# Performance work log

Hardware: AMD Instinct MI355X
Metric: run time of the kernel (lower is better)

The kernel has to match this reference:

```python
import jax, jax.numpy as jnp
import numpy as np
import math

B, S, D = 2, 2048, 512
H = 8
DEPTH = D // H
MAX_REL = 1024
NEG_INF = -1.0e9


def skew(t):
    # t: (..., r, c). Pad a zero column on the left, reshape to move relative
    # logits into their absolute positions (Music Transformer skew trick).
    r, c = t.shape[-2], t.shape[-1]
    padded = jnp.pad(t, [(0, 0)] * (t.ndim - 1) + [(1, 0)])
    s = padded.reshape(-1, c + 1, r)[:, 1:]
    return s.reshape(t.shape)


def setup_inputs() -> dict:
    key = jax.random.key(0)
    ks = jax.random.split(key, 12)
    sc = 1.0 / math.sqrt(D)
    return {
        "q": jax.random.normal(ks[0], (B, S, D), jnp.float32),
        "k": jax.random.normal(ks[1], (B, S, D), jnp.float32),
        "v": jax.random.normal(ks[2], (B, S, D), jnp.float32),
        "mask": jax.random.randint(ks[3], (B, 1, S, S), 0, 2, jnp.int32),
        "Wq_w": jax.random.normal(ks[4], (D, D), jnp.float32) * sc,
        "Wq_b": jnp.zeros((D,), jnp.float32),
        "Wk_w": jax.random.normal(ks[5], (D, D), jnp.float32) * sc,
        "Wk_b": jnp.zeros((D,), jnp.float32),
        "Wv_w": jax.random.normal(ks[6], (D, D), jnp.float32) * sc,
        "Wv_b": jnp.zeros((D,), jnp.float32),
        "E": jax.random.normal(ks[7], (MAX_REL, D), jnp.float32),
        "Wo_w": jax.random.normal(ks[8], (D, D), jnp.float32) * sc,
        "Wo_b": jnp.zeros((D,), jnp.float32),
    }


def reference(q, k, v, mask, Wq_w, Wq_b, Wk_w, Wk_b, Wv_w, Wv_b, E, Wo_w, Wo_b):
    # Linear projections (torch Linear: x @ W^T + b)
    qp = q @ Wq_w.T + Wq_b
    kp = k @ Wk_w.T + Wk_b
    vp = v @ Wv_w.T + Wv_b

    # Required relative position embeddings for seq_len S (S >= MAX_REL here:
    # repeat E[0] for the first S-MAX_REL positions, then the full table).
    n_rep = max(0, S - MAX_REL)
    e = jnp.concatenate([jnp.tile(E[0:1], (n_rep, 1)), E[max(0, MAX_REL - S):]], axis=0)  # (S, D)

    # Split heads: (B,S,D)->(B,H,S,depth); e: (S,D)->(H,S,depth)
    qh = qp.reshape(B, S, H, DEPTH).transpose(0, 2, 1, 3)
    kh = kp.reshape(B, S, H, DEPTH).transpose(0, 2, 1, 3)
    vh = vp.reshape(B, S, H, DEPTH).transpose(0, 2, 1, 3)
    eh = e.reshape(S, H, DEPTH).transpose(1, 0, 2)

    QKt = jnp.einsum('bhqd,bhkd->bhqk', qh, kh)
    Srel = skew(jnp.einsum('bhqd,hkd->bhqk', qh, eh))
    logits = (QKt + Srel) / math.sqrt(DEPTH)
    logits = logits + mask.astype(logits.dtype) * NEG_INF
    attn = jnp.einsum('bhqk,bhkd->bhqd', jax.nn.softmax(logits, axis=-1), vh)

    # Merge heads and output projection
    out = attn.transpose(0, 2, 1, 3).reshape(B, S, D)
    return out @ Wo_w.T + Wo_b
```

## Files before the change

### kernel.cpp

```cpp
#include <hip/hip_runtime.h>
#include <hip/hip_bf16.h>

#define BB 2
#define SS 2048
#define DD 512
#define HH 8
#define DP 64
#define MR 1024

typedef __attribute__((ext_vector_type(8))) short bf16x8;
typedef __attribute__((ext_vector_type(4))) float floatx4;

static __device__ __forceinline__ unsigned short f2b(float x) {
    __hip_bfloat16 h = __float2bfloat16(x);
    return *reinterpret_cast<unsigned short*>(&h);
}
static __device__ __forceinline__ float b2f(unsigned short u) {
    __hip_bfloat16 h = *reinterpret_cast<__hip_bfloat16*>(&u);
    return __bfloat162float(h);
}
static __device__ __forceinline__ unsigned int cvtpk(float lo, float hi) {
    unsigned int r;
    asm("v_cvt_pk_bf16_f32 %0, %1, %2" : "=v"(r) : "v"(lo), "v"(hi));
    return r;
}
static __device__ __forceinline__ void gll16(const void* g, void* l) {
    __builtin_amdgcn_global_load_lds(
        (const __attribute__((address_space(1))) void*)g,
        (__attribute__((address_space(3))) void*)l, 16, 0, 0);
}
static __device__ __forceinline__ int xoff(int ks, int quad, int row) {
    return (((ks * 4 + quad) ^ (row & 7)) * 16);
}

__global__ __launch_bounds__(256) void prep_kernel(
    const float* __restrict__ Wq, const float* __restrict__ Wk,
    const float* __restrict__ Wv, const float* __restrict__ Wo,
    const float* __restrict__ E,  const float* __restrict__ q,
    const float* __restrict__ k,  const float* __restrict__ v,
    const int* __restrict__ mask,
    unsigned short* __restrict__ Wqb, unsigned short* __restrict__ Wkb,
    unsigned short* __restrict__ Wvb, unsigned short* __restrict__ Wob,
    unsigned short* __restrict__ Eb,  unsigned short* __restrict__ qb16,
    unsigned short* __restrict__ kb16, unsigned short* __restrict__ vb16,
    unsigned long long* __restrict__ bits)
{
    const int blk = blockIdx.x;
    if (blk < 7680) {
        const int gid = blk * 256 + threadIdx.x;
        const float* src; unsigned short* dst; int off;
        if      (gid < 65536)   { src = Wq; dst = Wqb;  off = gid; }
        else if (gid < 131072)  { src = Wk; dst = Wkb;  off = gid - 65536; }
        else if (gid < 196608)  { src = Wv; dst = Wvb;  off = gid - 131072; }
        else if (gid < 262144)  { src = Wo; dst = Wob;  off = gid - 196608; }
        else if (gid < 393216)  { src = E;  dst = Eb;   off = gid - 262144; }
        else if (gid < 917504)  { src = q;  dst = qb16; off = gid - 393216; }
        else if (gid < 1441792) { src = k;  dst = kb16; off = gid - 917504; }
        else                    { src = v;  dst = vb16; off = gid - 1441792; }
        float4 x = ((const float4*)src)[off];
        ushort4 u; u.x = f2b(x.x); u.y = f2b(x.y); u.z = f2b(x.z); u.w = f2b(x.w);
        ((ushort4*)dst)[off] = u;
    } else {
        const size_t wid = (size_t)(blk - 7680) * 4 + (threadIdx.x >> 6);
        const int lane = threadIdx.x & 63;
        const int mv = mask[wid * 64 + lane];
        unsigned long long bal = __ballot(mv != 0);
        if (lane == 0) bits[wid] = bal;
    }
}

static __device__ __forceinline__ void gemm64_main(
    const unsigned short* __restrict__ A, const unsigned short* __restrict__ Wb,
    char* AsB, char* WsB, int m0, int n0,
    const int srow[2], const int scol[2],
    int w, int quad, int l15, int wm, int wn,
    floatx4 acc[2][2])
{
    for (int k0 = 0; k0 < 512; k0 += 64) {
        if (k0) __syncthreads();
#pragma unroll
        for (int i = 0; i < 2; i++) {
            gll16(A + (size_t)(m0 + srow[i]) * 512 + k0 + scol[i] * 8,
                  AsB + (w * 2 + i) * 1024);
            gll16(Wb + (size_t)(n0 + srow[i]) * 512 + k0 + scol[i] * 8,
                  WsB + (w * 2 + i) * 1024);
        }
        __syncthreads();
#pragma unroll
        for (int ks = 0; ks < 2; ks++) {
            bf16x8 a[2], bb[2];
#pragma unroll
            for (int mi = 0; mi < 2; mi++) {
                const int row = wm * 32 + mi * 16 + l15;
                a[mi] = *(const bf16x8*)(AsB + row * 128 + xoff(ks, quad, row));
            }
#pragma unroll
            for (int ni = 0; ni < 2; ni++) {
                const int row = wn * 32 + ni * 16 + l15;
                bb[ni] = *(const bf16x8*)(WsB + row * 128 + xoff(ks, quad, row));
            }
#pragma unroll
            for (int mi = 0; mi < 2; mi++)
#pragma unroll
                for (int ni = 0; ni < 2; ni++)
                    acc[mi][ni] = __builtin_amdgcn_mfma_f32_16x16x32_bf16(
                        a[mi], bb[ni], acc[mi][ni], 0, 0, 0);
        }
    }
}

__global__ __launch_bounds__(256) void gemm_proj(
    const unsigned short* __restrict__ Xq, const unsigned short* __restrict__ Xk,
    const unsigned short* __restrict__ Xv,
    const unsigned short* __restrict__ Wqb, const unsigned short* __restrict__ Wkb,
    const unsigned short* __restrict__ Wvb,
    const float* __restrict__ bq, const float* __restrict__ bk,
    const float* __restrict__ bv,
    const unsigned short* __restrict__ Eb,
    unsigned short* __restrict__ qp, unsigned short* __restrict__ kp,
    unsigned short* __restrict__ vpT, unsigned short* __restrict__ G)
{
    const int z = blockIdx.z;
    __shared__ __align__(16) char parena[27648];
    char* AsB = parena;
    char* WsB = parena + 8192;
    const int t = threadIdx.x, lane = t & 63, w = t >> 6;
    const int quad = lane >> 4, l15 = lane & 15;
    const int wm = w >> 1, wn = w & 1;
    const int m0 = blockIdx.x * 64, n0 = blockIdx.y * 64;

    int srow[2], scol[2];
#pragma unroll
    for (int i = 0; i < 2; i++) {
        const int p = (w * 2 + i) * 64 + lane;
        srow[i] = p >> 3; scol[i] = (p & 7) ^ (srow[i] & 7);
    }

    floatx4 acc[2][2];
#pragma unroll
    for (int mi = 0; mi < 2; mi++)
#pragma unroll
        for (int ni = 0; ni < 2; ni++)
            acc[mi][ni] = (floatx4){0.f, 0.f, 0.f, 0.f};

    if (z == 1) {
        gemm64_main(Xk, Wkb, AsB, WsB, m0, n0, srow, scol, w, quad, l15, wm, wn, acc);
#pragma unroll
        for (int ni = 0; ni < 2; ni++) {
            const int n = n0 + wn * 32 + ni * 16 + l15;
            const float bvl = bk[n];
#pragma unroll
            for (int mi = 0; mi < 2; mi++)
#pragma unroll
                for (int r = 0; r < 4; r++) {
                    const size_t m = (size_t)(m0 + wm * 32 + mi * 16 + quad * 4 + r);
                    kp[m * 512 + n] = f2b(acc[mi][ni][r] + bvl);
                }
        }
        __syncthreads();
#pragma unroll
        for (int mi = 0; mi < 2; mi++)
#pragma unroll
            for (int ni = 0; ni < 2; ni++)
                acc[mi][ni] = (floatx4){0.f, 0.f, 0.f, 0.f};
        gemm64_main(Xv, Wvb, AsB, WsB, m0, n0, srow, scol, w, quad, l15, wm, wn, acc);
        __syncthreads();
        unsigned short* Ls = (unsigned short*)parena;
#pragma unroll
        for (int ni = 0; ni < 2; ni++) {
            const int dcol = wn * 32 + ni * 16 + l15;
            const float bvl = bv[n0 + dcol];
#pragma unroll
            for (int mi = 0; mi < 2; mi++)
#pragma unroll
                for (int r = 0; r < 4; r++) {
                    const int srw = wm * 32 + mi * 16 + quad * 4 + r;
                    Ls[dcol * 72 + srw] = f2b(acc[mi][ni][r] + bvl);
                }
        }
        __syncthreads();
        const int bb2 = blockIdx.x >> 5, s0 = (blockIdx.x & 31) * 64, hh = blockIdx.y;
        const int drow = t >> 2, sc8 = (t & 3) * 8;
#pragma unroll
        for (int half = 0; half < 2; half++) {
            *(uint4*)&vpT[((size_t)(bb2 * 8 + hh) * 64 + drow) * SS + s0 + half * 32 + sc8] =
                *(const uint4*)&Ls[drow * 72 + half * 32 + sc8];
        }
    } else {
        gemm64_main(Xq, Wqb, AsB, WsB, m0, n0, srow, scol, w, quad, l15, wm, wn, acc);
        __syncthreads();
        unsigned short* Ls = (unsigned short*)parena;
#pragma unroll
        for (int ni = 0; ni < 2; ni++) {
            const int ch = wn * 32 + ni * 16 + l15;
            const float bvl = bq[n0 + ch];
#pragma unroll
            for (int mi = 0; mi < 2; mi++)
#pragma unroll
                for (int r = 0; r < 4; r++)
                    Ls[(wm * 32 + mi * 16 + quad * 4 + r) * 72 + ch] =
                        f2b(acc[mi][ni][r] + bvl);
        }
        __syncthreads();
        {
            const int row = t >> 2, c16 = (t & 3) * 16;
            const unsigned short* ls = &Ls[row * 72 + c16];
            unsigned short* qdst = &qp[(size_t)(m0 + row) * 512 + n0 + c16];
            *(uint4*)qdst = *(const uint4*)ls;
            *(uint4*)(qdst + 8) = *(const uint4*)(ls + 8);
        }
        bf16x8 af0 = *(const bf16x8*)&Ls[(w * 16 + l15) * 72 + quad * 8];
        bf16x8 af1 = *(const bf16x8*)&Ls[(w * 16 + l15) * 72 + 32 + quad * 8];

        const int bblk = m0 >> 11;
        const int i0 = m0 & 2047;
        const size_t grow0 = (size_t)(bblk * 8 + blockIdx.y) * SS + i0;
        char* EbL = parena + 10240;
        unsigned short* Gtw = (unsigned short*)(parena + 18432 + w * 2304);

        const int orow = lane >> 2, oseg = lane & 3;

        for (int tc = 0; tc < 16; tc++) {
            if (tc) __syncthreads();
#pragma unroll
            for (int i = 0; i < 2; i++)
                gll16(Eb + (size_t)(tc * 64 + srow[i]) * 512 + n0 + scol[i] * 8,
                      EbL + (w * 2 + i) * 1024);
            __syncthreads();
#pragma unroll
            for (int tt = 0; tt < 4; tt++) {
                const int row = tt * 16 + l15;
                bf16x8 b0 = *(const bf16x8*)(EbL + row * 128 + xoff(0, quad, row));
                bf16x8 b1 = *(const bf16x8*)(EbL + row * 128 + xoff(1, quad, row));
                floatx4 a2 = (floatx4){0.f, 0.f, 0.f, 0.f};
                a2 = __builtin_amdgcn_mfma_f32_16x16x32_bf16(af0, b0, a2, 0, 0, 0);
                a2 = __builtin_amdgcn_mfma_f32_16x16x32_bf16(af1, b1, a2, 0, 0, 0);
#pragma unroll
                for (int r = 0; r < 4; r++)
                    Gtw[(quad * 4 + r) * 72 + tt * 16 + l15] = f2b(a2[r]);
            }
            const unsigned short* gsrc = &Gtw[orow * 72 + oseg * 16];
            unsigned short* gdst = &G[(grow0 + w * 16 + orow) * MR + tc * 64 + oseg * 16];
            *(uint4*)gdst = *(const uint4*)gsrc;
            *(uint4*)(gdst + 8) = *(const uint4*)(gsrc + 8);
        }
    }
}

__global__ __launch_bounds__(256) void gemm_out(
    const unsigned short* __restrict__ A, const unsigned short* __restrict__ Wb,
    const float* __restrict__ bias, float* __restrict__ Out)
{
    __shared__ __align__(16) char parena[16384];
    char* AsB = parena;
    char* WsB = parena + 8192;
    const int t = threadIdx.x, lane = t & 63, w = t >> 6;
    const int quad = lane >> 4, l15 = lane & 15;
    const int wm = w >> 1, wn = w & 1;
    const int m0 = blockIdx.x * 64, n0 = blockIdx.y * 64;

    int srow[2], scol[2];
#pragma unroll
    for (int i = 0; i < 2; i++) {
        const int p = (w * 2 + i) * 64 + lane;
        srow[i] = p >> 3; scol[i] = (p & 7) ^ (srow[i] & 7);
    }

    floatx4 acc[2][2];
#pragma unroll
    for (int mi = 0; mi < 2; mi++)
#pragma unroll
        for (int ni = 0; ni < 2; ni++)
            acc[mi][ni] = (floatx4){0.f, 0.f, 0.f, 0.f};

    gemm64_main(A, Wb, AsB, WsB, m0, n0, srow, scol, w, quad, l15, wm, wn, acc);

#pragma unroll
    for (int ni = 0; ni < 2; ni++) {
        const int n = n0 + wn * 32 + ni * 16 + l15;
        const float bvl = bias[n];
#pragma unroll
        for (int mi = 0; mi < 2; mi++)
#pragma unroll
            for (int r = 0; r < 4; r++) {
                const size_t m = (size_t)(m0 + wm * 32 + mi * 16 + quad * 4 + r);
                Out[m * 512 + n] = acc[mi][ni][r] + bvl;
            }
    }
}

struct RelPF { ushort4 hi; ushort4 lo; int path; };

static __device__ __forceinline__ void rel_issue(
    const unsigned short* __restrict__ pdiag, int i0w, int k0, int quad,
    RelPF pf[2])
{
#pragma unroll
    for (int ct = 0; ct < 2; ct++) {
        const int k0c = k0 + ct * 16;
        const int gj0 = k0c + quad * 4;
        const int dmax = i0w + 15 - k0c;
        const int dmin = i0w - (k0c + 15);
        int path;
        if (dmin >= MR) path = 0;
        else if (dmin >= 0 && dmax <= MR - 1) path = 1;
        else if (dmax <= -2 && dmin >= -(MR + 1)) path = 2;
        else if (dmax <= -(MR + 2)) path = 3;
        else path = 4;
        pf[ct].path = path;
        if (path == 1 || path == 4) {
            const unsigned short* p = pdiag + 1023 + gj0;
            pf[ct].hi.x = p[0]; pf[ct].hi.y = p[1];
            pf[ct].hi.z = p[2]; pf[ct].hi.w = p[3];
        }
        if (path == 3 || path == 4) {
            const unsigned short* p = pdiag + max(gj0 - 2, 0);
            pf[ct].lo.x = p[0]; pf[ct].lo.y = p[1];
            pf[ct].lo.z = p[2]; pf[ct].lo.w = p[3];
        }
    }
}

static __device__ __forceinline__ void rel_convert(
    const RelPF& pf, int gi, int k0c, int quad,
    float d0a, float d0b, float relc[4])
{
    const int path = pf.path;
    if (path == 0) {
        relc[0] = relc[1] = relc[2] = relc[3] = d0a;
    } else if (path == 1) {
        relc[0] = b2f(pf.hi.x); relc[1] = b2f(pf.hi.y);
        relc[2] = b2f(pf.hi.z); relc[3] = b2f(pf.hi.w);
    } else if (path == 2) {
        relc[0] = relc[1] = relc[2] = relc[3] = d0b;
    } else if (path == 3) {
        relc[0] = b2f(pf.lo.x); relc[1] = b2f(pf.lo.y);
        relc[2] = b2f(pf.lo.z); relc[3] = b2f(pf.lo.w);
    } else {
        const int gj0 = k0c + quad * 4;
        const unsigned short hv[4] = {pf.hi.x, pf.hi.y, pf.hi.z, pf.hi.w};
        const unsigned short lv[4] = {pf.lo.x, pf.lo.y, pf.lo.z, pf.lo.w};
#pragma unroll
        for (int r = 0; r < 4; r++) {
            const int dd = gi - (gj0 + r);
            float rl;
            if (dd >= MR) rl = d0a;
            else if (dd >= 0) rl = b2f(hv[r]);
            else if (dd == -1) rl = 0.0f;
            else if (dd >= -(MR + 1)) rl = d0b;
            else rl = b2f(lv[r]);
            relc[r] = rl;
        }
    }
}

__global__ __launch_bounds__(256, 4) void attn_kernel(
    const unsigned short* __restrict__ qp, const unsigned short* __restrict__ kp,
    const unsigned short* __restrict__ vpT, const unsigned int* __restrict__ mb32,
    const unsigned short* __restrict__ G, unsigned short* __restrict__ ao)
{
    __shared__ __align__(16) char smem[38016];
    const int t = threadIdx.x, lane = t & 63, w = t >> 6;
    const int quad = lane >> 4, l15 = lane & 15;
    const int wr = w >> 1, kh = w & 1;
    const int bh = blockIdx.y, b = bh >> 3, h = bh & 7;
    const int i0w = blockIdx.x * 32 + wr * 16;
    const int gi = i0w + l15;

    const unsigned short* kb = kp + (size_t)b * SS * DD + h * DP;
    const unsigned short* vb = vpT + (size_t)bh * DP * SS;
    const unsigned short* Gb = G + (size_t)bh * SS * MR;
    const unsigned int* mrow32 = mb32 + ((size_t)b * SS + gi) * 64;

    const unsigned short* qrow = qp + ((size_t)b * SS + gi) * DD + h * DP;
    bf16x8 qf0 = *(const bf16x8*)(qrow + quad * 8);
    bf16x8 qf1 = *(const bf16x8*)(qrow + 32 + quad * 8);

    const unsigned short* pdiag = Gb + (size_t)gi * 1023;
    const float d0a = b2f(Gb[(size_t)gi * MR]);
    const float d0b = b2f(Gb[(size_t)min(gi + 1, SS - 1) * MR]);

    char* Kh = smem + kh * 8192;
    char* Vh = smem + 16384 + kh * 8192;
    char* Pt = smem + 32768 + w * 1280;

    int kofs[2], vofs[2], dst[2];
#pragma unroll
    for (int i = 0; i < 2; i++) {
        const int c = wr * 2 + i;
        const int p = c * 64 + lane;
        const int krow = p >> 3, kcol = (p & 7) ^ (krow & 7);
        kofs[i] = krow * DD + kcol * 8;
        const int vrow = p >> 2, vcol = (p & 3) ^ (vrow & 3);
        vofs[i] = vrow * SS + vcol * 8;
        dst[i] = c * 1024;
    }

    floatx4 oacc[4];
#pragma unroll
    for (int ct = 0; ct < 4; ct++) oacc[ct] = (floatx4){0.f, 0.f, 0.f, 0.f};
    float lsum = 0.0f;

    {
        const int k0 = kh * 1024;
        gll16(kb + (size_t)k0 * DD + kofs[0], Kh + dst[0]);
        gll16(kb + (size_t)k0 * DD + kofs[1], Kh + dst[1]);
        gll16(vb + k0 + vofs[0], Vh + dst[0]);
        gll16(vb + k0 + vofs[1], Vh + dst[1]);
    }
    unsigned int mwv = mrow32[kh * 32];
    RelPF pf[2];
    rel_issue(pdiag, i0w, kh * 1024, quad, pf);

    const float C1 = 0.125f * 1.4426950408889634f;
    const float C2 = -18.75f * 1.4426950408889634f;

    for (int it = 0; it < 32; it++) {
        const int cur = it & 1;
        __syncthreads();
        if (it + 1 < 32) {
            const int k0n = kh * 1024 + (it + 1) * 32;
            const int nb = (cur ^ 1) * 4096;
            gll16(kb + (size_t)k0n * DD + kofs[0], Kh + nb + dst[0]);
            gll16(kb + (size_t)k0n * DD + kofs[1], Kh + nb + dst[1]);
            gll16(vb + k0n + vofs[0], Vh + nb + dst[0]);
            gll16(vb + k0n + vofs[1], Vh + nb + dst[1]);
        }
        const unsigned int mcur = mwv;

        float relc[2][4];
        rel_convert(pf[0], gi, kh * 1024 + it * 32,      quad, d0a, d0b, relc[0]);
        rel_convert(pf[1], gi, kh * 1024 + it * 32 + 16, quad, d0a, d0b, relc[1]);

        {
            const int itn = (it + 1 < 32) ? it + 1 : 31;
            mwv = mrow32[kh * 32 + itn];
            rel_issue(pdiag, i0w, kh * 1024 + itn * 32, quad, pf);
        }

        char* Kc = Kh + cur * 4096;
        char* Vc = Vh + cur * 4096;

        bf16x8 kf[2][2];
#pragma unroll
        for (int ct = 0; ct < 2; ct++) {
            const int row = ct * 16 + l15;
            kf[ct][0] = *(const bf16x8*)(Kc + row * 128 + ((quad ^ (l15 & 7)) * 16));
            kf[ct][1] = *(const bf16x8*)(Kc + row * 128 + (((4 + quad) ^ (l15 & 7)) * 16));
        }
        bf16x8 vf[4];
#pragma unroll
        for (int ct = 0; ct < 4; ct++) {
            const int drow = ct * 16 + l15;
            vf[ct] = *(const bf16x8*)(Vc + drow * 64 + ((quad ^ (drow & 3)) * 16));
        }

        floatx4 acc[2];
#pragma unroll
        for (int ct = 0; ct < 2; ct++) {
            const unsigned int nib = (mcur >> (ct * 16 + quad * 4)) & 0xFu;
            floatx4 a;
#pragma unroll
            for (int r = 0; r < 4; r++)
                a[r] = relc[ct][r] + (((nib >> r) & 1u) ? -8.0e9f : 0.0f);
            acc[ct] = a;
        }
        __builtin_amdgcn_s_setprio(1);
#pragma unroll
        for (int ct = 0; ct < 2; ct++) {
            acc[ct] = __builtin_amdgcn_mfma_f32_16x16x32_bf16(kf[ct][0], qf0, acc[ct], 0, 0, 0);
            acc[ct] = __builtin_amdgcn_mfma_f32_16x16x32_bf16(kf[ct][1], qf1, acc[ct], 0, 0, 0);
        }
        __builtin_amdgcn_s_setprio(0);

#pragma unroll
        for (int ct = 0; ct < 2; ct++) {
            const float p0 = __builtin_exp2f(fmaf(acc[ct][0], C1, C2));
            const float p1 = __builtin_exp2f(fmaf(acc[ct][1], C1, C2));
            const float p2 = __builtin_exp2f(fmaf(acc[ct][2], C1, C2));
            const float p3 = __builtin_exp2f(fmaf(acc[ct][3], C1, C2));
            lsum += (p0 + p1) + (p2 + p3);
            uint2 u;
            u.x = cvtpk(p0, p1);
            u.y = cvtpk(p2, p3);
            *(uint2*)(Pt + l15 * 80 + ct * 32 + quad * 8) = u;
        }

        bf16x8 pt = *(const bf16x8*)(Pt + l15 * 80 + quad * 16);
        __builtin_amdgcn_s_setprio(1);
#pragma unroll
        for (int ct = 0; ct < 4; ct++)
            oacc[ct] = __builtin_amdgcn_mfma_f32_16x16x32_bf16(vf[ct], pt, oacc[ct], 0, 0, 0);
        __builtin_amdgcn_s_setprio(0);
    }

    lsum += __shfl_xor(lsum, 16);
    lsum += __shfl_xor(lsum, 32);

    __syncthreads();
    float* OmW = (float*)(smem + wr * 4352);
    float* MlW = (float*)(smem + 37888);
    if (kh == 1) {
#pragma unroll
        for (int ct = 0; ct < 4; ct++)
            *(floatx4*)&OmW[l15 * 68 + ct * 16 + quad * 4] = oacc[ct];
        if (lane < 16) MlW[wr * 16 + lane] = lsum;
    }
    __syncthreads();
    if (kh == 0) {
        const float inv = 1.0f / (lsum + MlW[wr * 16 + l15]);
#pragma unroll
        for (int ct = 0; ct < 4; ct++) {
            floatx4 o1 = *(const floatx4*)&OmW[l15 * 68 + ct * 16 + quad * 4];
            ushort4 u;
            u.x = f2b((oacc[ct][0] + o1[0]) * inv);
            u.y = f2b((oacc[ct][1] + o1[1]) * inv);
            u.z = f2b((oacc[ct][2] + o1[2]) * inv);
            u.w = f2b((oacc[ct][3] + o1[3]) * inv);
            *(ushort4*)&ao[((size_t)b * SS + gi) * DD + h * DP + ct * 16 + quad * 4] = u;
        }
    }
}

extern "C" void kernel_launch(void* const* d_in, const int* in_sizes, int n_in,
                              void* d_out, int out_size, void* d_ws, size_t ws_size,
                              hipStream_t stream)
{
    const float* q    = (const float*)d_in[0];
    const float* k    = (const float*)d_in[1];
    const float* v    = (const float*)d_in[2];
    const int*   mask = (const int*)d_in[3];
    const float* Wq_w = (const float*)d_in[4];
    const float* Wq_b = (const float*)d_in[5];
    const float* Wk_w = (const float*)d_in[6];
    const float* Wk_b = (const float*)d_in[7];
    const float* Wv_w = (const float*)d_in[8];
    const float* Wv_b = (const float*)d_in[9];
    const float* E    = (const float*)d_in[10];
    const float* Wo_w = (const float*)d_in[11];
    const float* Wo_b = (const float*)d_in[12];
    float* out = (float*)d_out;

    char* ws = (char*)d_ws;
    unsigned short* G    = (unsigned short*)ws;
    unsigned short* qp   = (unsigned short*)(ws + 67108864);
    unsigned short* kp   = qp + 2097152;
    unsigned short* vpT  = kp + 2 * 2097152;
    unsigned short* qb16 = vpT + 2097152;
    unsigned short* kb16 = qb16 + 2097152;
    unsigned short* vb16 = kb16 + 2097152;
    unsigned short* aob  = qb16;
    unsigned long long* mbits = (unsigned long long*)(ws + 67108864 + 7 * 4194304);
    unsigned short* Wqb = (unsigned short*)(ws + 67108864 + 7 * 4194304 + 1048576);
    unsigned short* Wkb = Wqb + 262144;
    unsigned short* Wvb = Wkb + 262144;
    unsigned short* Wob = Wvb + 262144;
    unsigned short* Ebf = Wob + 262144;

    dim3 blk(256);
    hipLaunchKernelGGL(prep_kernel, dim3(40448), blk, 0, stream,
                       Wq_w, Wk_w, Wv_w, Wo_w, E, q, k, v, mask,
                       Wqb, Wkb, Wvb, Wob, Ebf, qb16, kb16, vb16, mbits);
    hipLaunchKernelGGL(gemm_proj, dim3(64, 8, 2), blk, 0, stream,
                       qb16, kb16, vb16, Wqb, Wkb, Wvb, Wq_b, Wk_b, Wv_b,
                       Ebf, qp, kp, vpT, G);
    hipLaunchKernelGGL(attn_kernel, dim3(64, 16), blk, 0, stream,
                       qp, kp, vpT, (const unsigned int*)mbits, G, aob);
    hipLaunchKernelGGL(gemm_out, dim3(64, 8), blk, 0, stream, aob, Wob, Wo_b, out);
}
```

Baseline: 224.2 us.

## Move mask bitpacking and Wo conversion into extra z-slice of projection GEMM

The mask ballot bit-packing and the Wo fp32-to-bf16 conversion are removed from the prep kernel and run in a third z-slice of the projection GEMM grid. Those bandwidth-heavy blocks (mask is 32 MB of int32) can then run alongside the compute-bound GEMM blocks, shortening the prep kernel. The cost is that each z=2 block loops over 64 ballot iterations, so the longer tail may hurt GEMM scheduling.

```diff
diff --git a/kernel.cpp b/kernel.cpp
--- a/kernel.cpp
+++ b/kernel.cpp
@@ -35,38 +35,26 @@
 
 __global__ __launch_bounds__(256) void prep_kernel(
     const float* __restrict__ Wq, const float* __restrict__ Wk,
-    const float* __restrict__ Wv, const float* __restrict__ Wo,
-    const float* __restrict__ E,  const float* __restrict__ q,
-    const float* __restrict__ k,  const float* __restrict__ v,
-    const int* __restrict__ mask,
+    const float* __restrict__ Wv, const float* __restrict__ E,
+    const float* __restrict__ q,  const float* __restrict__ k,
+    const float* __restrict__ v,
     unsigned short* __restrict__ Wqb, unsigned short* __restrict__ Wkb,
-    unsigned short* __restrict__ Wvb, unsigned short* __restrict__ Wob,
-    unsigned short* __restrict__ Eb,  unsigned short* __restrict__ qb16,
-    unsigned short* __restrict__ kb16, unsigned short* __restrict__ vb16,
-    unsigned long long* __restrict__ bits)
-{
-    const int blk = blockIdx.x;
-    if (blk < 7680) {
-        const int gid = blk * 256 + threadIdx.x;
-        const float* src; unsigned short* dst; int off;
-        if      (gid < 65536)   { src = Wq; dst = Wqb;  off = gid; }
-        else if (gid < 131072)  { src = Wk; dst = Wkb;  off = gid - 65536; }
-        else if (gid < 196608)  { src = Wv; dst = Wvb;  off = gid - 131072; }
-        else if (gid < 262144)  { src = Wo; dst = Wob;  off = gid - 196608; }
-        else if (gid < 393216)  { src = E;  dst = Eb;   off = gid - 262144; }
-        else if (gid < 917504)  { src = q;  dst = qb16; off = gid - 393216; }
-        else if (gid < 1441792) { src = k;  dst = kb16; off = gid - 917504; }
-        else                    { src = v;  dst = vb16; off = gid - 1441792; }
-        float4 x = ((const float4*)src)[off];
-        ushort4 u; u.x = f2b(x.x); u.y = f2b(x.y); u.z = f2b(x.z); u.w = f2b(x.w);
-        ((ushort4*)dst)[off] = u;
-    } else {
-        const size_t wid = (size_t)(blk - 7680) * 4 + (threadIdx.x >> 6);
-        const int lane = threadIdx.x & 63;
-        const int mv = mask[wid * 64 + lane];
-        unsigned long long bal = __ballot(mv != 0);
-        if (lane == 0) bits[wid] = bal;
-    }
+    unsigned short* __restrict__ Wvb, unsigned short* __restrict__ Eb,
+    unsigned short* __restrict__ qb16, unsigned short* __restrict__ kb16,
+    unsigned short* __restrict__ vb16)
+{
+    const int gid = blockIdx.x * 256 + threadIdx.x;
+    const float* src; unsigned short* dst; int off;
+    if      (gid < 65536)   { src = Wq; dst = Wqb;  off = gid; }
+    else if (gid < 131072)  { src = Wk; dst = Wkb;  off = gid - 65536; }
+    else if (gid < 196608)  { src = Wv; dst = Wvb;  off = gid - 131072; }
+    else if (gid < 327680)  { src = E;  dst = Eb;   off = gid - 196608; }
+    else if (gid < 851968)  { src = q;  dst = qb16; off = gid - 327680; }
+    else if (gid < 1376256) { src = k;  dst = kb16; off = gid - 851968; }
+    else                    { src = v;  dst = vb16; off = gid - 1376256; }
+    float4 x = ((const float4*)src)[off];
+    ushort4 u; u.x = f2b(x.x); u.y = f2b(x.y); u.z = f2b(x.z); u.w = f2b(x.w);
+    ((ushort4*)dst)[off] = u;
 }
 
 static __device__ __forceinline__ void gemm64_main(
@@ -117,14 +105,35 @@
     const float* __restrict__ bq, const float* __restrict__ bk,
     const float* __restrict__ bv,
     const unsigned short* __restrict__ Eb,
+    const float* __restrict__ Wo, const int* __restrict__ mask,
     unsigned short* __restrict__ qp, unsigned short* __restrict__ kp,
-    unsigned short* __restrict__ vpT, unsigned short* __restrict__ G)
+    unsigned short* __restrict__ vpT, unsigned short* __restrict__ G,
+    unsigned short* __restrict__ Wob, unsigned long long* __restrict__ bits)
 {
     const int z = blockIdx.z;
+    const int t = threadIdx.x, lane = t & 63, w = t >> 6;
+
+    if (z == 2) {
+        const int bid = blockIdx.y * 64 + blockIdx.x;
+        if (t < 128) {
+            const int gid = bid * 128 + t;
+            float4 x = ((const float4*)Wo)[gid];
+            ushort4 u; u.x = f2b(x.x); u.y = f2b(x.y); u.z = f2b(x.z); u.w = f2b(x.w);
+            ((ushort4*)Wob)[gid] = u;
+        }
+#pragma unroll 4
+        for (int i = 0; i < 64; i++) {
+            const size_t wid = (size_t)bid * 256 + i * 4 + w;
+            const int mv = mask[wid * 64 + lane];
+            unsigned long long bal = __ballot(mv != 0);
+            if (lane == 0) bits[wid] = bal;
+        }
+        return;
+    }
+
     __shared__ __align__(16) char parena[27648];
     char* AsB = parena;
     char* WsB = parena + 8192;
-    const int t = threadIdx.x, lane = t & 63, w = t >> 6;
     const int quad = lane >> 4, l15 = lane & 15;
     const int wm = w >> 1, wn = w & 1;
     const int m0 = blockIdx.x * 64, n0 = blockIdx.y * 64;
@@ -558,12 +567,12 @@
     unsigned short* Ebf = Wob + 262144;
 
     dim3 blk(256);
-    hipLaunchKernelGGL(prep_kernel, dim3(40448), blk, 0, stream,
-                       Wq_w, Wk_w, Wv_w, Wo_w, E, q, k, v, mask,
-                       Wqb, Wkb, Wvb, Wob, Ebf, qb16, kb16, vb16, mbits);
-    hipLaunchKernelGGL(gemm_proj, dim3(64, 8, 2), blk, 0, stream,
+    hipLaunchKernelGGL(prep_kernel, dim3(7424), blk, 0, stream,
+                       Wq_w, Wk_w, Wv_w, E, q, k, v,
+                       Wqb, Wkb, Wvb, Ebf, qb16, kb16, vb16);
+    hipLaunchKernelGGL(gemm_proj, dim3(64, 8, 3), blk, 0, stream,
                        qb16, kb16, vb16, Wqb, Wkb, Wvb, Wq_b, Wk_b, Wv_b,
-                       Ebf, qp, kp, vpT, G);
+                       Ebf, Wo_w, mask, qp, kp, vpT, G, Wob, mbits);
     hipLaunchKernelGGL(attn_kernel, dim3(64, 16), blk, 0, stream,
                        qp, kp, vpT, (const unsigned int*)mbits, G, aob);
     hipLaunchKernelGGL(gemm_out, dim3(64, 8), blk, 0, stream, aob, Wob, Wo_b, out);
```

After: 250.9 us. 11.9% more time.
